# Performance work log

Hardware: AMD Instinct MI355X
Metric: run time of the kernel (lower is better)

Reference implementation:

```python
import jax, jax.numpy as jnp
import numpy as np

H = 4  # attention heads for the single degree-0 fiber

def _layer_norm(x, gamma):
    mu = x.mean(-1, keepdims=True)
    var = ((x - mu) ** 2).mean(-1, keepdims=True)
    return (x - mu) / jnp.sqrt(var + 1e-5) * gamma

def _silu(x):
    return x * jax.nn.sigmoid(x)

def _forward(features, rel_dist, norm_scale, Wq, Wxi, Wxj,
             rp_W1, rp_b1, rp_g1, rp_W2, rp_b2, rp_g2, rp_W3, rp_b3,
             Wkv_out, Wout, neighbor_indices, neighbor_mask):
    b, n, d, _ = features.shape
    k = neighbor_indices.shape[-1]
    hid = Wq.shape[1]
    dh = hid // H
    kvd = Wkv_out.shape[0]
    scale = dh ** -0.5

    # ---- prenorm: RMS (over feature channels) of per-m L2 norms; m=1 for degree 0
    rms = jnp.sqrt(jnp.sum(features ** 2, axis=-2, keepdims=True)) * (d ** -0.5)
    x = features / jnp.maximum(rms, 1e-12) * norm_scale      # (b,n,d,1)
    x = x[..., 0]                                            # (b,n,d)

    # ---- queries
    q = x @ Wq                                               # (b,n,hid)

    # ---- DTP to_kv (degree0->degree0): project xi/xj, gather neighbors, radial kernel
    xi = x @ Wxi
    xj = x @ Wxj
    xg = jax.vmap(lambda t, idx: t[idx])(xj, neighbor_indices)   # (b,n,k,d)
    xe = xg + xi[:, :, None, :]

    hdd = _layer_norm(_silu(rel_dist @ rp_W1 + rp_b1), rp_g1)    # (b,n,k,rh)
    hdd = _layer_norm(_silu(hdd @ rp_W2 + rp_b2), rp_g2)
    R = (hdd @ rp_W3 + rp_b3).reshape(b, n, k, kvd, d)           # per-edge (lo,li) kernel
    kv = jnp.einsum('bnkod,bnkd->bnko', R, xe)                   # (b,n,k,kvd)
    kv = kv @ Wkv_out                                            # DTP project_out
    kk, vv = jnp.split(kv, 2, axis=-1)                           # (b,n,k,hid) each

    # ---- L2-distance attention over neighbors
    qh = q.reshape(b, n, H, dh).transpose(0, 2, 1, 3)            # (b,h,n,dh)
    kh = kk.reshape(b, n, k, H, dh).transpose(0, 3, 1, 2, 4)     # (b,h,n,k,dh)
    vh = vv.reshape(b, n, k, H, dh).transpose(0, 3, 1, 2, 4)
    diff = qh[:, :, :, None, :] - kh + 1e-6                      # F.pairwise_distance eps
    sim = -jnp.sqrt(jnp.sum(diff * diff, axis=-1)) * scale       # (b,h,n,k)
    sim = jnp.where(neighbor_mask[:, None], sim, -jnp.finfo(sim.dtype).max)
    attn = jax.nn.softmax(sim, axis=-1)
    out = jnp.einsum('bhnk,bhnkd->bhnd', attn, vh)
    out = out.transpose(0, 2, 1, 3).reshape(b, n, hid)

    return (out @ Wout)[..., None]                               # (b,n,d,1)

def setup_inputs() -> dict:
    key = jax.random.key(0)
    ks = jax.random.split(key, 16)
    b, n, k, d = 2, 256, 16, 64
    hid = H * 32           # heads * dim_head = 128
    kvd = 2 * hid          # 256
    rh = 64                # radial_hidden_dim
    rnd = lambda i, shape, s=1.0: jax.random.normal(ks[i], shape, jnp.float32) * s
    return dict(
        features=rnd(0, (b, n, d, 1)),
        neighbor_indices=jax.random.randint(ks[1], (b, n, k), 0, n),
        neighbor_mask=jax.random.bernoulli(ks[2], 0.9, (b, n, k)),
        rel_dist=jax.random.uniform(ks[3], (b, n, k, 1), jnp.float32),
        norm_scale=jnp.ones((d, 1), jnp.float32),
        Wq=rnd(4, (d, hid), d ** -0.5),
        Wxi=rnd(5, (d, d), d ** -0.5),
        Wxj=rnd(6, (d, d), d ** -0.5),
        rp_W1=rnd(7, (1, rh)), rp_b1=jnp.zeros((rh,), jnp.float32),
        rp_g1=jnp.ones((rh,), jnp.float32),
        rp_W2=rnd(8, (rh, rh), rh ** -0.5), rp_b2=jnp.zeros((rh,), jnp.float32),
        rp_g2=jnp.ones((rh,), jnp.float32),
        rp_W3=rnd(9, (rh, kvd * d), rh ** -0.5), rp_b3=jnp.zeros((kvd * d,), jnp.float32),
        Wkv_out=rnd(10, (kvd, kvd), kvd ** -0.5),
        Wout=rnd(11, (hid, d), hid ** -0.5),
    )

def reference(features, neighbor_indices, neighbor_mask, rel_dist, norm_scale,
              Wq, Wxi, Wxj, rp_W1, rp_b1, rp_g1, rp_W2, rp_b2, rp_g2,
              rp_W3, rp_b3, Wkv_out, Wout):
    return _forward(features, rel_dist, norm_scale, Wq, Wxi, Wxj,
                    rp_W1, rp_b1, rp_g1, rp_W2, rp_b2, rp_g2, rp_W3, rp_b3,
                    Wkv_out, Wout, neighbor_indices, neighbor_mask)
```

## Files before the change

kernel.cpp:

```cpp
#include <hip/hip_runtime.h>
#include <hip/hip_bf16.h>
#include <float.h>

#define BB 2
#define NN 256
#define DD 64
#define KK 16
#define NH 4
#define HID 128
#define KVD 256
#define RH 64
#define NNODES (BB*NN)
#define NEDGES (NNODES*KK)

typedef unsigned int uint32;
typedef unsigned short ushort_t;
typedef float f32x4_t __attribute__((ext_vector_type(4)));
typedef short bf16x8_t __attribute__((ext_vector_type(8)));
typedef __attribute__((address_space(3))) ushort_t lds_us;
typedef __attribute__((address_space(1))) const ushort_t glb_us;

__device__ __forceinline__ uint32 cvtpk_bf16(float lo, float hi) {
  uint32 r;
  asm("v_cvt_pk_bf16_f32 %0, %1, %2" : "=v"(r) : "v"(lo), "v"(hi));
  return r;
}

__device__ __forceinline__ float wave_sum64(float v) {
  #pragma unroll
  for (int m = 32; m; m >>= 1) v += __shfl_xor(v, m, 64);
  return v;
}
__device__ __forceinline__ float grp32_sum(float v) {
  #pragma unroll
  for (int m = 16; m; m >>= 1) v += __shfl_xor(v, m, 64);
  return v;
}

__global__ __launch_bounds__(256) void node_w3_kernel(
    const float* __restrict__ feat, const float* __restrict__ gscale,
    const float* __restrict__ Wq, const float* __restrict__ Wxi,
    const float* __restrict__ Wxj,
    const float* __restrict__ W3, const float* __restrict__ b3,
    float* __restrict__ q_ws, float* __restrict__ xi_ws, float* __restrict__ xj_ws,
    ushort_t* __restrict__ W3bf) {
  int bx = blockIdx.x;
  if (bx >= 128) {
    const int W3N = 64 * KVD * DD;
    int i = ((bx - 128) * 256 + threadIdx.x) * 8;
    const float* src = (i < W3N) ? (W3 + i) : (b3 + (i - W3N));
    float4 a = ((const float4*)src)[0];
    float4 b = ((const float4*)src)[1];
    float v[8] = {a.x, a.y, a.z, a.w, b.x, b.y, b.z, b.w};
    union { uint4 q; ushort_t s[8]; } o;
    #pragma unroll
    for (int jj = 0; jj < 8; ++jj) {
      uint32 u = __float_as_uint(v[jj]);
      o.s[jj] = (ushort_t)((u + 0x7FFFu + ((u >> 16) & 1u)) >> 16);
    }
    int rr = i >> 14, j0 = i & 16383;
    int oc = j0 >> 6, gr = (j0 >> 3) & 7;
    int byte_sw = oc * 128 + ((gr * 16) ^ ((oc & 7) << 4));
    *(uint4*)(W3bf + (rr << 14) + (byte_sw >> 1)) = o.q;
    return;
  }
  int sub = threadIdx.x >> 6;
  int t = threadIdx.x & 63;
  int node = bx * 4 + sub;
  __shared__ float xs[4][DD];
  float f = feat[node * DD + t];
  float ss = wave_sum64(f * f);
  float rms = sqrtf(ss) * 0.125f;
  float den = fmaxf(rms, 1e-12f);
  float x = f / den * gscale[t];
  xs[sub][t] = x;
  __syncthreads();
  float q0 = 0.f, q1 = 0.f, xiv = 0.f, xjv = 0.f;
  #pragma unroll 4
  for (int d = 0; d < DD; ++d) {
    float xv = xs[sub][d];
    q0  += xv * Wq[d * HID + t];
    q1  += xv * Wq[d * HID + 64 + t];
    xiv += xv * Wxi[d * DD + t];
    xjv += xv * Wxj[d * DD + t];
  }
  q_ws[node * HID + t] = q0;
  q_ws[node * HID + 64 + t] = q1;
  xi_ws[node * DD + t] = xiv;
  xj_ws[node * DD + t] = xjv;
}

__global__ __launch_bounds__(64) void edge_kernel(
    const int* __restrict__ nbi, const float* __restrict__ rel,
    const float* __restrict__ W1, const float* __restrict__ b1,
    const float* __restrict__ g1, const float* __restrict__ W2,
    const float* __restrict__ b2, const float* __restrict__ g2,
    const float* __restrict__ xi_ws, const float* __restrict__ xj_ws,
    float* __restrict__ h2_ws, float* __restrict__ xe_ws) {
  int e = blockIdx.x;
  int t = threadIdx.x;
  int node = e >> 4;
  int j = e & 15;
  int bb = node >> 8;
  __shared__ float hs[RH];
  float rd = rel[e];
  float h = rd * W1[t] + b1[t];
  h = h / (1.f + expf(-h));
  float mu = wave_sum64(h) * (1.f / RH);
  float c = h - mu;
  float var = wave_sum64(c * c) * (1.f / RH);
  float xn = c * rsqrtf(var + 1e-5f) * g1[t];
  hs[t] = xn;
  __syncthreads();
  float p = b2[t];
  #pragma unroll 4
  for (int r = 0; r < RH; ++r) p += hs[r] * W2[r * RH + t];
  p = p / (1.f + expf(-p));
  mu = wave_sum64(p) * (1.f / RH);
  c = p - mu;
  var = wave_sum64(c * c) * (1.f / RH);
  float h2v = c * rsqrtf(var + 1e-5f) * g2[t];
  h2_ws[e * RH + t] = h2v;
  int nb = nbi[node * KK + j];
  xe_ws[e * DD + t] = xj_ws[(bb * NN + nb) * DD + t] + xi_ws[node * DD + t];
}

#define AFRAG(dst, base, h) {                                     \
  union { bf16x8_t v; uint32 u[4]; } t_;                          \
  t_.u[0] = cvtpk_bf16(xf[(base)+0]*(h), xf[(base)+1]*(h));       \
  t_.u[1] = cvtpk_bf16(xf[(base)+2]*(h), xf[(base)+3]*(h));       \
  t_.u[2] = cvtpk_bf16(xf[(base)+4]*(h), xf[(base)+5]*(h));       \
  t_.u[3] = cvtpk_bf16(xf[(base)+6]*(h), xf[(base)+7]*(h));       \
  dst = t_.v; }

__global__ __launch_bounds__(256) void kv_kernel(
    const ushort_t* __restrict__ W3bf,
    const float* __restrict__ h2_ws, const float* __restrict__ xe_ws,
    float* __restrict__ kv_ws) {
  int bx = blockIdx.x;
  int eb = bx >> 2, ob = bx & 3;
  int o0 = ob * 64;
  int tid = threadIdx.x;
  int we = tid >> 6, l = tid & 63;
  int l15 = l & 15, g = l >> 4;
  int ebase = eb * 64;
  __shared__ float h2_s[64 * 68];
  __shared__ ushort_t bstage[2][2][4096];
  {
    int row = tid >> 2, c0 = (tid & 3) * 16;
    const float* src = h2_ws + (ebase + row) * RH + c0;
    float* dst = &h2_s[row * 68 + c0];
    #pragma unroll
    for (int q = 0; q < 4; ++q) ((float4*)dst)[q] = ((const float4*)src)[q];
  }
  int erow = ebase + we * 16 + l15;
  const float* xsrc = xe_ws + erow * DD + g * 8;
  float xf[16];
  #pragma unroll
  for (int jj = 0; jj < 8; ++jj) { xf[jj] = xsrc[jj]; xf[8 + jj] = xsrc[32 + jj]; }

  #define STAGE(buf, r0_) {                                                   \
    int ra_ = ((r0_) > 64) ? 64 : (r0_);                                      \
    int rb_ = ((r0_) + 1 > 64) ? 64 : ((r0_) + 1);                            \
    const ushort_t* sa_ = W3bf + ((size_t)ra_ << 14) + o0 * 64;               \
    const ushort_t* sb_ = W3bf + ((size_t)rb_ << 14) + o0 * 64;               \
    ushort_t* da_ = &bstage[buf][0][0];                                       \
    ushort_t* db_ = &bstage[buf][1][0];                                       \
    __builtin_amdgcn_global_load_lds((glb_us*)(sa_ + tid * 8),        (lds_us*)(da_ + tid * 8), 16, 0, 0);        \
    __builtin_amdgcn_global_load_lds((glb_us*)(sa_ + 2048 + tid * 8), (lds_us*)(da_ + 2048 + tid * 8), 16, 0, 0); \
    __builtin_amdgcn_global_load_lds((glb_us*)(sb_ + tid * 8),        (lds_us*)(db_ + tid * 8), 16, 0, 0);        \
    __builtin_amdgcn_global_load_lds((glb_us*)(sb_ + 2048 + tid * 8), (lds_us*)(db_ + 2048 + tid * 8), 16, 0, 0); }

  STAGE(0, 0);
  asm volatile("s_waitcnt vmcnt(0)" ::: "memory");
  __syncthreads();

  int e68 = (we * 16 + l15) * 68;
  int swz = (l15 & 7) << 4;
  f32x4_t acc0 = {0,0,0,0}, acc1 = {0,0,0,0}, acc2 = {0,0,0,0}, acc3 = {0,0,0,0};
  int cur = 0;
  for (int p = 0; p < 33; ++p) {
    int r0 = 2 * p;
    if (p < 32) STAGE(cur ^ 1, r0 + 2);
    #pragma unroll
    for (int rl = 0; rl < 2; ++rl) {
      int r = r0 + rl;
      if (r > 64) break;
      const char* bp = (const char*)&bstage[cur][rl][0];
      bf16x8_t bf0 = *(const bf16x8_t*)(bp + l15*128 +    0 + ((g*16)     ^ swz));
      bf16x8_t bf1 = *(const bf16x8_t*)(bp + l15*128 +    0 + (((4+g)*16) ^ swz));
      bf16x8_t bf2 = *(const bf16x8_t*)(bp + l15*128 + 2048 + ((g*16)     ^ swz));
      bf16x8_t bf3 = *(const bf16x8_t*)(bp + l15*128 + 2048 + (((4+g)*16) ^ swz));
      bf16x8_t bf4 = *(const bf16x8_t*)(bp + l15*128 + 4096 + ((g*16)     ^ swz));
      bf16x8_t bf5 = *(const bf16x8_t*)(bp + l15*128 + 4096 + (((4+g)*16) ^ swz));
      bf16x8_t bf6 = *(const bf16x8_t*)(bp + l15*128 + 6144 + ((g*16)     ^ swz));
      bf16x8_t bf7 = *(const bf16x8_t*)(bp + l15*128 + 6144 + (((4+g)*16) ^ swz));
      float h = (r < 64) ? h2_s[e68 + r] : 1.0f;
      bf16x8_t a0, a1;
      AFRAG(a0, 0, h); AFRAG(a1, 8, h);
      acc0 = __builtin_amdgcn_mfma_f32_16x16x32_bf16(a0, bf0, acc0, 0, 0, 0);
      acc0 = __builtin_amdgcn_mfma_f32_16x16x32_bf16(a1, bf1, acc0, 0, 0, 0);
      acc1 = __builtin_amdgcn_mfma_f32_16x16x32_bf16(a0, bf2, acc1, 0, 0, 0);
      acc1 = __builtin_amdgcn_mfma_f32_16x16x32_bf16(a1, bf3, acc1, 0, 0, 0);
      acc2 = __builtin_amdgcn_mfma_f32_16x16x32_bf16(a0, bf4, acc2, 0, 0, 0);
      acc2 = __builtin_amdgcn_mfma_f32_16x16x32_bf16(a1, bf5, acc2, 0, 0, 0);
      acc3 = __builtin_amdgcn_mfma_f32_16x16x32_bf16(a0, bf6, acc3, 0, 0, 0);
      acc3 = __builtin_amdgcn_mfma_f32_16x16x32_bf16(a1, bf7, acc3, 0, 0, 0);
    }
    asm volatile("s_waitcnt vmcnt(0)" ::: "memory");
    __syncthreads();
    cur ^= 1;
  }
  int orow = (ebase + we * 16 + g * 4) * KVD + o0 + l15;
  #pragma unroll
  for (int q = 0; q < 4; ++q) {
    kv_ws[orow + q * KVD +  0] = acc0[q];
    kv_ws[orow + q * KVD + 16] = acc1[q];
    kv_ws[orow + q * KVD + 32] = acc2[q];
    kv_ws[orow + q * KVD + 48] = acc3[q];
  }
}

__global__ __launch_bounds__(128) void attn_kernel(
    const float* __restrict__ q_ws, const float* __restrict__ kv_ws,
    const int* __restrict__ maskp, const float* __restrict__ Wkv,
    const float* __restrict__ Wout, float* __restrict__ out) {
  int node = blockIdx.x;
  int t = threadIdx.x;
  int h = t >> 5;
  __shared__ float kvs[KK * 260];
  __shared__ float sim_s[NH * KK];
  __shared__ float o_s[HID];
  {
    int e = t >> 3, c0 = (t & 7) * 32;
    const float* src = kv_ws + (node * KK + e) * KVD + c0;
    float* dst = &kvs[e * 260 + c0];
    #pragma unroll
    for (int q = 0; q < 8; ++q) ((float4*)dst)[q] = ((const float4*)src)[q];
  }
  __syncthreads();
  float kk2[KK] = {}, vv2[KK] = {};
  #pragma unroll 4
  for (int k = 0; k < KVD; ++k) {
    float w1 = Wkv[k * KVD + t];
    float w2 = Wkv[k * KVD + 128 + t];
    #pragma unroll
    for (int e = 0; e < KK; ++e) {
      float kvv = kvs[e * 260 + k];
      kk2[e] += kvv * w1;
      vv2[e] += kvv * w2;
    }
  }
  float qv = q_ws[node * HID + t];
  const float scale = 0.17677669529663689f;
  #pragma unroll
  for (int j = 0; j < KK; ++j) {
    float diff = qv - kk2[j] + 1e-6f;
    float s = grp32_sum(diff * diff);
    if ((t & 31) == 0) sim_s[h * KK + j] = -sqrtf(s) * scale;
  }
  __syncthreads();
  float sv[KK];
  float m = -FLT_MAX;
  #pragma unroll
  for (int j = 0; j < KK; ++j) {
    bool msk = maskp[node * KK + j] != 0;
    float s = msk ? sim_s[h * KK + j] : -FLT_MAX;
    sv[j] = s;
    m = fmaxf(m, s);
  }
  float sum = 0.f, wv[KK];
  #pragma unroll
  for (int j = 0; j < KK; ++j) { wv[j] = expf(sv[j] - m); sum += wv[j]; }
  float inv = 1.f / sum;
  float ot = 0.f;
  #pragma unroll
  for (int j = 0; j < KK; ++j) ot += wv[j] * vv2[j];
  o_s[t] = ot * inv;
  __syncthreads();
  if (t < DD) {
    float r = 0.f;
    #pragma unroll 4
    for (int cI = 0; cI < HID; ++cI) r += o_s[cI] * Wout[cI * DD + t];
    out[node * DD + t] = r;
  }
}

extern "C" void kernel_launch(void* const* d_in, const int* in_sizes, int n_in,
                              void* d_out, int out_size, void* d_ws, size_t ws_size,
                              hipStream_t stream) {
  const float* feat = (const float*)d_in[0];
  const int*   nbi  = (const int*)d_in[1];
  const int*   msk  = (const int*)d_in[2];
  const float* rel  = (const float*)d_in[3];
  const float* gsc  = (const float*)d_in[4];
  const float* Wq   = (const float*)d_in[5];
  const float* Wxi  = (const float*)d_in[6];
  const float* Wxj  = (const float*)d_in[7];
  const float* W1   = (const float*)d_in[8];
  const float* b1   = (const float*)d_in[9];
  const float* g1   = (const float*)d_in[10];
  const float* W2   = (const float*)d_in[11];
  const float* b2   = (const float*)d_in[12];
  const float* g2   = (const float*)d_in[13];
  const float* W3   = (const float*)d_in[14];
  const float* b3   = (const float*)d_in[15];
  const float* Wkv  = (const float*)d_in[16];
  const float* Wout = (const float*)d_in[17];

  float* ws      = (float*)d_ws;
  float* q_ws    = ws;
  float* xi_ws   = q_ws  + NNODES * HID;
  float* xj_ws   = xi_ws + NNODES * DD;
  float* h2_ws   = xj_ws + NNODES * DD;
  float* xe_ws   = h2_ws + NEDGES * RH;
  float* kv_ws   = xe_ws + NEDGES * DD;
  ushort_t* W3bf = (ushort_t*)(kv_ws + NEDGES * KVD);

  node_w3_kernel<<<648, 256, 0, stream>>>(feat, gsc, Wq, Wxi, Wxj, W3, b3,
                                          q_ws, xi_ws, xj_ws, W3bf);
  edge_kernel<<<NEDGES, 64, 0, stream>>>(nbi, rel, W1, b1, g1, W2, b2, g2,
                                         xi_ws, xj_ws, h2_ws, xe_ws);
  kv_kernel<<<512, 256, 0, stream>>>(W3bf, h2_ws, xe_ws, kv_ws);
  attn_kernel<<<NNODES, 128, 0, stream>>>(q_ws, kv_ws, msk, Wkv, Wout,
                                          (float*)d_out);
}
```

Before: 185.8 us.

## Use bf16 MFMA for Wkv_out projection in attention kernel

The attention kernel's fp32 scalar matmul of per-edge kv (16x256) by Wkv_out (256x256) is replaced by bf16 MFMA 16x16x32 instructions. kv rows are converted to bf16 in registers, and Wkv_out is pre-transposed and converted to bf16 by extra blocks in the first kernel. The softmax over neighbors is reorganized around the MFMA accumulator layout using wave shuffles, with one wave computing attention weights and the other applying them to values. This lowers ALU and LDS cost per node but brings bf16 rounding into the key and value projections.

Result: faster. 164.2 us (-11.6%).

```diff
diff --git a/kernel.cpp b/kernel.cpp
--- a/kernel.cpp
+++ b/kernel.cpp
@@ -31,10 +31,10 @@
   for (int m = 32; m; m >>= 1) v += __shfl_xor(v, m, 64);
   return v;
 }
-__device__ __forceinline__ float grp32_sum(float v) {
-  #pragma unroll
-  for (int m = 16; m; m >>= 1) v += __shfl_xor(v, m, 64);
-  return v;
+
+__device__ __forceinline__ ushort_t rne_bf16(float f) {
+  uint32 u = __float_as_uint(f);
+  return (ushort_t)((u + 0x7FFFu + ((u >> 16) & 1u)) >> 16);
 }
 
 __global__ __launch_bounds__(256) void node_w3_kernel(
@@ -42,9 +42,19 @@
     const float* __restrict__ Wq, const float* __restrict__ Wxi,
     const float* __restrict__ Wxj,
     const float* __restrict__ W3, const float* __restrict__ b3,
+    const float* __restrict__ Wkv,
     float* __restrict__ q_ws, float* __restrict__ xi_ws, float* __restrict__ xj_ws,
-    ushort_t* __restrict__ W3bf) {
+    ushort_t* __restrict__ W3bf, ushort_t* __restrict__ Wkvt) {
   int bx = blockIdx.x;
+  if (bx >= 648) {
+    int i = ((bx - 648) * 256 + threadIdx.x) * 4;
+    int n = i >> 8, k0 = i & 255;
+    union { uint2 q; ushort_t s[4]; } o;
+    #pragma unroll
+    for (int j = 0; j < 4; ++j) o.s[j] = rne_bf16(Wkv[(k0 + j) * KVD + n]);
+    *(uint2*)(Wkvt + n * KVD + k0) = o.q;
+    return;
+  }
   if (bx >= 128) {
     const int W3N = 64 * KVD * DD;
     int i = ((bx - 128) * 256 + threadIdx.x) * 8;
@@ -54,10 +64,7 @@
     float v[8] = {a.x, a.y, a.z, a.w, b.x, b.y, b.z, b.w};
     union { uint4 q; ushort_t s[8]; } o;
     #pragma unroll
-    for (int jj = 0; jj < 8; ++jj) {
-      uint32 u = __float_as_uint(v[jj]);
-      o.s[jj] = (ushort_t)((u + 0x7FFFu + ((u >> 16) & 1u)) >> 16);
-    }
+    for (int jj = 0; jj < 8; ++jj) o.s[jj] = rne_bf16(v[jj]);
     int rr = i >> 14, j0 = i & 16383;
     int oc = j0 >> 6, gr = (j0 >> 3) & 7;
     int byte_sw = oc * 128 + ((gr * 16) ^ ((oc & 7) << 4));
@@ -223,66 +230,103 @@
 
 __global__ __launch_bounds__(128) void attn_kernel(
     const float* __restrict__ q_ws, const float* __restrict__ kv_ws,
-    const int* __restrict__ maskp, const float* __restrict__ Wkv,
+    const int* __restrict__ maskp, const ushort_t* __restrict__ Wkvt,
     const float* __restrict__ Wout, float* __restrict__ out) {
   int node = blockIdx.x;
-  int t = threadIdx.x;
-  int h = t >> 5;
-  __shared__ float kvs[KK * 260];
-  __shared__ float sim_s[NH * KK];
+  int tid = threadIdx.x;
+  int w = tid >> 6, l = tid & 63;
+  int l15 = l & 15, g = l >> 4;
+  __shared__ float attn_s[NH * KK];
   __shared__ float o_s[HID];
+  bf16x8_t a[8];
   {
-    int e = t >> 3, c0 = (t & 7) * 32;
-    const float* src = kv_ws + (node * KK + e) * KVD + c0;
-    float* dst = &kvs[e * 260 + c0];
-    #pragma unroll
-    for (int q = 0; q < 8; ++q) ((float4*)dst)[q] = ((const float4*)src)[q];
-  }
-  __syncthreads();
-  float kk2[KK] = {}, vv2[KK] = {};
-  #pragma unroll 4
-  for (int k = 0; k < KVD; ++k) {
-    float w1 = Wkv[k * KVD + t];
-    float w2 = Wkv[k * KVD + 128 + t];
-    #pragma unroll
-    for (int e = 0; e < KK; ++e) {
-      float kvv = kvs[e * 260 + k];
-      kk2[e] += kvv * w1;
-      vv2[e] += kvv * w2;
-    }
-  }
-  float qv = q_ws[node * HID + t];
+    const float* kvrow = kv_ws + (size_t)(node * KK + l15) * KVD + g * 8;
+    #pragma unroll
+    for (int c = 0; c < 8; ++c) {
+      union { bf16x8_t v; uint32 u[4]; } t_;
+      t_.u[0] = cvtpk_bf16(kvrow[c*32 + 0], kvrow[c*32 + 1]);
+      t_.u[1] = cvtpk_bf16(kvrow[c*32 + 2], kvrow[c*32 + 3]);
+      t_.u[2] = cvtpk_bf16(kvrow[c*32 + 4], kvrow[c*32 + 5]);
+      t_.u[3] = cvtpk_bf16(kvrow[c*32 + 6], kvrow[c*32 + 7]);
+      a[c] = t_.v;
+    }
+  }
+  f32x4_t acc[8];
+  #pragma unroll
+  for (int nt = 0; nt < 8; ++nt) {
+    acc[nt] = (f32x4_t){0.f, 0.f, 0.f, 0.f};
+    const ushort_t* bbase = Wkvt + (size_t)(w * 128 + nt * 16 + l15) * KVD + g * 8;
+    #pragma unroll
+    for (int c = 0; c < 8; ++c) {
+      bf16x8_t b = *(const bf16x8_t*)(bbase + c * 32);
+      acc[nt] = __builtin_amdgcn_mfma_f32_16x16x32_bf16(a[c], b, acc[nt], 0, 0, 0);
+    }
+  }
   const float scale = 0.17677669529663689f;
-  #pragma unroll
-  for (int j = 0; j < KK; ++j) {
-    float diff = qv - kk2[j] + 1e-6f;
-    float s = grp32_sum(diff * diff);
-    if ((t & 31) == 0) sim_s[h * KK + j] = -sqrtf(s) * scale;
-  }
-  __syncthreads();
-  float sv[KK];
-  float m = -FLT_MAX;
-  #pragma unroll
-  for (int j = 0; j < KK; ++j) {
-    bool msk = maskp[node * KK + j] != 0;
-    float s = msk ? sim_s[h * KK + j] : -FLT_MAX;
-    sv[j] = s;
-    m = fmaxf(m, s);
-  }
-  float sum = 0.f, wv[KK];
-  #pragma unroll
-  for (int j = 0; j < KK; ++j) { wv[j] = expf(sv[j] - m); sum += wv[j]; }
-  float inv = 1.f / sum;
-  float ot = 0.f;
-  #pragma unroll
-  for (int j = 0; j < KK; ++j) ot += wv[j] * vv2[j];
-  o_s[t] = ot * inv;
-  __syncthreads();
-  if (t < DD) {
+  if (w == 0) {
+    float sim[4][4];
+    #pragma unroll
+    for (int h = 0; h < 4; ++h) {
+      #pragma unroll
+      for (int q = 0; q < 4; ++q) {
+        float s = 0.f;
+        #pragma unroll
+        for (int p = 0; p < 2; ++p) {
+          int nt = h * 2 + p;
+          float qv = q_ws[node * HID + nt * 16 + l15];
+          float diff = qv - acc[nt][q] + 1e-6f;
+          s += diff * diff;
+        }
+        #pragma unroll
+        for (int m = 8; m; m >>= 1) s += __shfl_xor(s, m, 64);
+        sim[q][h] = -sqrtf(s) * scale;
+      }
+    }
+    int mv[4];
+    #pragma unroll
+    for (int q = 0; q < 4; ++q) mv[q] = maskp[node * KK + g * 4 + q];
+    #pragma unroll
+    for (int h = 0; h < 4; ++h) {
+      float sv[4];
+      float mx = -FLT_MAX;
+      #pragma unroll
+      for (int q = 0; q < 4; ++q) {
+        sv[q] = mv[q] ? sim[q][h] : -FLT_MAX;
+        mx = fmaxf(mx, sv[q]);
+      }
+      mx = fmaxf(mx, __shfl_xor(mx, 16, 64));
+      mx = fmaxf(mx, __shfl_xor(mx, 32, 64));
+      float se = 0.f, ev[4];
+      #pragma unroll
+      for (int q = 0; q < 4; ++q) { ev[q] = expf(sv[q] - mx); se += ev[q]; }
+      se += __shfl_xor(se, 16, 64);
+      se += __shfl_xor(se, 32, 64);
+      float inv = 1.f / se;
+      if (l15 == 0) {
+        #pragma unroll
+        for (int q = 0; q < 4; ++q) attn_s[h * KK + g * 4 + q] = ev[q] * inv;
+      }
+    }
+  }
+  __syncthreads();
+  if (w == 1) {
+    #pragma unroll
+    for (int nt = 0; nt < 8; ++nt) {
+      int h = nt >> 1;
+      float o = 0.f;
+      #pragma unroll
+      for (int q = 0; q < 4; ++q) o += attn_s[h * KK + g * 4 + q] * acc[nt][q];
+      o += __shfl_xor(o, 16, 64);
+      o += __shfl_xor(o, 32, 64);
+      if (g == 0) o_s[nt * 16 + l15] = o;
+    }
+  }
+  __syncthreads();
+  if (tid < DD) {
     float r = 0.f;
     #pragma unroll 4
-    for (int cI = 0; cI < HID; ++cI) r += o_s[cI] * Wout[cI * DD + t];
-    out[node * DD + t] = r;
+    for (int cI = 0; cI < HID; ++cI) r += o_s[cI] * Wout[cI * DD + tid];
+    out[node * DD + tid] = r;
   }
 }
 
@@ -316,12 +360,13 @@
   float* xe_ws   = h2_ws + NEDGES * RH;
   float* kv_ws   = xe_ws + NEDGES * DD;
   ushort_t* W3bf = (ushort_t*)(kv_ws + NEDGES * KVD);
-
-  node_w3_kernel<<<648, 256, 0, stream>>>(feat, gsc, Wq, Wxi, Wxj, W3, b3,
-                                          q_ws, xi_ws, xj_ws, W3bf);
+  ushort_t* Wkvt = W3bf + 65 * 16384;
+
+  node_w3_kernel<<<712, 256, 0, stream>>>(feat, gsc, Wq, Wxi, Wxj, W3, b3, Wkv,
+                                          q_ws, xi_ws, xj_ws, W3bf, Wkvt);
   edge_kernel<<<NEDGES, 64, 0, stream>>>(nbi, rel, W1, b1, g1, W2, b2, g2,
                                          xi_ws, xj_ws, h2_ws, xe_ws);
   kv_kernel<<<512, 256, 0, stream>>>(W3bf, h2_ws, xe_ws, kv_ws);
-  attn_kernel<<<NNODES, 128, 0, stream>>>(q_ws, kv_ws, msk, Wkv, Wout,
+  attn_kernel<<<NNODES, 128, 0, stream>>>(q_ws, kv_ws, msk, Wkvt, Wout,
                                           (float*)d_out);
 }
```
